# Optimization experiments

Hardware: AMD Instinct MI355X
Metric: run time of the kernel (lower is better)

## Reference

```python
import jax, jax.numpy as jnp
import numpy as np

N_NODES = 10000
N_EDGES = 80000
LATENT = 128
OUT_SIZE = 3
NODE_F = 12
EDGE_F = 7
STEPS = 15
LN_EPS = 1e-5


def _mlp(x, W0, b0, W1, b1, W2, b2):
    h = jax.nn.relu(x @ W0 + b0)
    h = jax.nn.relu(h @ W1 + b1)
    return h @ W2 + b2


def _ln(x, g, b):
    m = jnp.mean(x, axis=-1, keepdims=True)
    v = jnp.mean(jnp.square(x - m), axis=-1, keepdims=True)
    return (x - m) * jax.lax.rsqrt(v + LN_EPS) * g + b


def _forward(node_features, edge_features, senders, receivers,
             enW0, enb0, enW1, enb1, enW2, enb2, eng, enbe,
             eeW0, eeb0, eeW1, eeb1, eeW2, eeb2, eeg, eebe,
             beW0, beb0, beW1, beb1, beW2, beb2, beg, bebe,
             bnW0, bnb0, bnW1, bnb1, bnW2, bnb2, bng, bnbe,
             dW0, db0, dW1, db1, dW2, db2):
    # Encoder: node and mesh-edge MLPs with LayerNorm
    nl = _ln(_mlp(node_features, enW0, enb0, enW1, enb1, enW2, enb2), eng, enbe)  # [N, L]
    el = _ln(_mlp(edge_features, eeW0, eeb0, eeW1, eeb1, eeW2, eeb2), eeg, eebe)  # [E, L]

    # Processor: 15 GraphNetBlocks with residual connections, scanned over stacked params
    def block(carry, p):
        n, e = carry
        (eW0, eb0, eW1, eb1, eW2, eb2, eg, ebe,
         nW0, nb0, nW1, nb1, nW2, nb2, ng, nbe) = p
        feat = jnp.concatenate([n[senders], n[receivers], e], axis=-1)  # [E, 3L]
        new_e = _ln(_mlp(feat, eW0, eb0, eW1, eb1, eW2, eb2), eg, ebe)  # [E, L]
        agg = jax.ops.segment_sum(new_e, receivers, num_segments=N_NODES)  # [N, L]
        new_n = _ln(_mlp(jnp.concatenate([n, agg], axis=-1), nW0, nb0, nW1, nb1, nW2, nb2), ng, nbe)
        return (n + new_n, e + new_e), None

    xs = (beW0, beb0, beW1, beb1, beW2, beb2, beg, bebe,
          bnW0, bnb0, bnW1, bnb1, bnW2, bnb2, bng, bnbe)
    (nl, el), _ = jax.lax.scan(jax.checkpoint(block), (nl, el), xs)

    # Decoder: MLP without LayerNorm
    return _mlp(nl, dW0, db0, dW1, db1, dW2, db2)  # [N, OUT_SIZE]


def setup_inputs() -> dict:
    ks = iter(jax.random.split(jax.random.key(0), 32))

    def W(*shape):
        return jax.random.normal(next(ks), shape, jnp.float32) * (1.0 / np.sqrt(shape[-2]))

    z = lambda *s: jnp.zeros(s, jnp.float32)
    o = lambda *s: jnp.ones(s, jnp.float32)
    d = {}
    d['node_features'] = jax.random.normal(next(ks), (N_NODES, NODE_F), jnp.float32)
    d['edge_features'] = jax.random.normal(next(ks), (N_EDGES, EDGE_F), jnp.float32)
    d['senders'] = jax.random.randint(next(ks), (N_EDGES,), 0, N_NODES, jnp.int32)
    d['receivers'] = jax.random.randint(next(ks), (N_EDGES,), 0, N_NODES, jnp.int32)
    d.update(enW0=W(NODE_F, LATENT), enb0=z(LATENT), enW1=W(LATENT, LATENT), enb1=z(LATENT),
             enW2=W(LATENT, LATENT), enb2=z(LATENT), eng=o(LATENT), enbe=z(LATENT))
    d.update(eeW0=W(EDGE_F, LATENT), eeb0=z(LATENT), eeW1=W(LATENT, LATENT), eeb1=z(LATENT),
             eeW2=W(LATENT, LATENT), eeb2=z(LATENT), eeg=o(LATENT), eebe=z(LATENT))
    d.update(beW0=W(STEPS, 3 * LATENT, LATENT), beb0=z(STEPS, LATENT),
             beW1=W(STEPS, LATENT, LATENT), beb1=z(STEPS, LATENT),
             beW2=W(STEPS, LATENT, LATENT), beb2=z(STEPS, LATENT),
             beg=o(STEPS, LATENT), bebe=z(STEPS, LATENT))
    d.update(bnW0=W(STEPS, 2 * LATENT, LATENT), bnb0=z(STEPS, LATENT),
             bnW1=W(STEPS, LATENT, LATENT), bnb1=z(STEPS, LATENT),
             bnW2=W(STEPS, LATENT, LATENT), bnb2=z(STEPS, LATENT),
             bng=o(STEPS, LATENT), bnbe=z(STEPS, LATENT))
    d.update(dW0=W(LATENT, LATENT), db0=z(LATENT), dW1=W(LATENT, LATENT), db1=z(LATENT),
             dW2=W(LATENT, OUT_SIZE), db2=z(OUT_SIZE))
    return d


def reference(node_features, edge_features, senders, receivers,
              enW0, enb0, enW1, enb1, enW2, enb2, eng, enbe,
              eeW0, eeb0, eeW1, eeb1, eeW2, eeb2, eeg, eebe,
              beW0, beb0, beW1, beb1, beW2, beb2, beg, bebe,
              bnW0, bnb0, bnW1, bnb1, bnW2, bnb2, bng, bnbe,
              dW0, db0, dW1, db1, dW2, db2):
    return _forward(node_features, edge_features, senders, receivers,
                    enW0, enb0, enW1, enb1, enW2, enb2, eng, enbe,
                    eeW0, eeb0, eeW1, eeb1, eeW2, eeb2, eeg, eebe,
                    beW0, beb0, beW1, beb1, beW2, beb2, beg, bebe,
                    bnW0, bnb0, bnW1, bnb1, bnW2, bnb2, bng, bnbe,
                    dW0, db0, dW1, db1, dW2, db2)
```

## Files before the change

### kernel.cpp

```cpp
#include <hip/hip_runtime.h>
#include <hip/hip_bf16.h>
#include <stdint.h>

#define N_NODES 10000
#define N_EDGES 80000
#define L 128
#define STEPS 15
#define LN_EPS 1e-5f
#define NTHR 256
#define H_STRIDE 272

typedef short short8 __attribute__((ext_vector_type(8)));
typedef float floatx4 __attribute__((ext_vector_type(4)));

__device__ __forceinline__ float bf2f(const __hip_bfloat16 x) {
    return __bfloat162float(x);
}
__device__ __forceinline__ float ldmix(const void* p, int idx, int isf32) {
    return isf32 ? ((const float*)p)[idx]
                 : bf2f(((const __hip_bfloat16*)p)[idx]);
}

__global__ void detect_dtype(const uint32_t* __restrict__ nf, int* cnt) {
    int c = 0;
    for (int i = blockIdx.x * blockDim.x + threadIdx.x; i < 60000;
         i += gridDim.x * blockDim.x) {
        const uint32_t w = nf[i];
        c += (((w >> 7) & 0xFF) >= 0xC6) + (((w >> 23) & 0xFF) >= 0xC6);
    }
    atomicAdd(cnt, c);
}

#define N_TMATS 14
struct TAll {
    const void* src[N_TMATS];
    long long cum[N_TMATS + 1];
    int K[N_TMATS], N[N_TMATS], Kpad[N_TMATS];
};

__global__ void transpose_all(TAll a, const int* __restrict__ cnt,
                              __hip_bfloat16* __restrict__ pool) {
    const int isf32 = (*cnt > 1000);
    const long long total = a.cum[N_TMATS];
    for (long long i = blockIdx.x * (long long)blockDim.x + threadIdx.x;
         i < total; i += gridDim.x * (long long)blockDim.x) {
        int e = 0;
        #pragma unroll 1
        for (int j = 1; j < N_TMATS; j++) if (i >= a.cum[j]) e = j;
        const long long r = i - a.cum[e];
        const int per = a.N[e] * a.Kpad[e];
        const int m = (int)(r / per);
        int r2 = (int)(r - (long long)m * per);
        const int c2   = r2 >> 12;
        const int rem  = r2 & 4095;
        const int ct   = rem >> 9;
        const int lane = (rem >> 3) & 63;
        const int j    = rem & 7;
        const int k    = c2 * 32 + (lane >> 4) * 8 + j;
        const int col  = ct * 16 + (lane & 15);
        float v = 0.f;
        if (k < a.K[e]) v = ldmix(a.src[e], (m * a.K[e] + k) * a.N[e] + col, isf32);
        pool[i] = __float2bfloat16(v);
    }
}

__global__ void convert_feats(const void* __restrict__ nf,
                              const void* __restrict__ ef,
                              const int* __restrict__ cnt,
                              const int* __restrict__ elist,
                              __hip_bfloat16* __restrict__ fN,
                              __hip_bfloat16* __restrict__ fE)
{
    const int isf32 = (*cnt > 1000);
    const int totN = N_NODES * 32;
    const int totE = N_EDGES * 32;
    for (int i = blockIdx.x * blockDim.x + threadIdx.x; i < totN + totE;
         i += gridDim.x * blockDim.x) {
        if (i < totN) {
            const int r = i >> 5, c = i & 31;
            fN[i] = __float2bfloat16(c < 12 ? ldmix(nf, r * 12 + c, isf32) : 0.f);
        } else {
            const int j = i - totN;
            const int r = j >> 5, c = j & 31;
            const int e = elist[r];
            fE[j] = __float2bfloat16(c < 7 ? ldmix(ef, e * 7 + c, isf32) : 0.f);
        }
    }
}

__global__ void csr_hist(const int* __restrict__ rcv, int* __restrict__ deg) {
    for (int i = blockIdx.x * blockDim.x + threadIdx.x; i < N_EDGES;
         i += gridDim.x * blockDim.x)
        atomicAdd(&deg[rcv[i]], 1);
}

__global__ void csr_scan(const int* __restrict__ deg, int* __restrict__ rowptr,
                         int* __restrict__ cursor) {
    __shared__ int part[256];
    __shared__ int partx[257];
    const int t = threadIdx.x;
    int s = 0;
    for (int j = 0; j < 40; j++) {
        const int i = t * 40 + j;
        if (i < N_NODES) s += deg[i];
    }
    part[t] = s;
    __syncthreads();
    if (t == 0) {
        int r = 0;
        for (int k = 0; k < 256; k++) { partx[k] = r; r += part[k]; }
        partx[256] = r;
    }
    __syncthreads();
    int run = partx[t];
    for (int j = 0; j < 40; j++) {
        const int i = t * 40 + j;
        if (i < N_NODES) {
            rowptr[i] = run;
            cursor[i] = run;
            run += deg[i];
        }
    }
    if (t == 255) rowptr[N_NODES] = partx[256];
}

__global__ void csr_scatter(const int* __restrict__ rcv, int* __restrict__ cursor,
                            int* __restrict__ elist) {
    for (int i = blockIdx.x * blockDim.x + threadIdx.x; i < N_EDGES;
         i += gridDim.x * blockDim.x) {
        const int p = atomicAdd(&cursor[rcv[i]], 1);
        elist[p] = i;
    }
}

__global__ void sort_meta(const int* __restrict__ snd, const int* __restrict__ rcv,
                          const int* __restrict__ elist,
                          int* __restrict__ ssnd, int* __restrict__ srcv) {
    for (int i = blockIdx.x * blockDim.x + threadIdx.x; i < N_EDGES;
         i += gridDim.x * blockDim.x) {
        const int e = elist[i];
        ssnd[i] = snd[e];
        srcv[i] = rcv[e];
    }
}

__global__ __launch_bounds__(256)
void csr_agg(const int* __restrict__ rowptr,
             const __hip_bfloat16* __restrict__ ln16,
             __hip_bfloat16* __restrict__ agg16)
{
    const int g = threadIdx.x >> 5;
    const int lane = threadIdx.x & 31;
    const int v = blockIdx.x * 8 + g;
    if (v >= N_NODES) return;
    const int c0 = lane * 4;
    float s0 = 0.f, s1 = 0.f, s2 = 0.f, s3 = 0.f;
    int j = rowptr[v];
    const int en = rowptr[v + 1];
    for (; j + 1 < en; j += 2) {
        union { uint2 w; __hip_bfloat16 h[4]; } u0, u1;
        u0.w = *(const uint2*)(ln16 + (size_t)j * L + c0);
        u1.w = *(const uint2*)(ln16 + (size_t)(j + 1) * L + c0);
        s0 += bf2f(u0.h[0]); s1 += bf2f(u0.h[1]); s2 += bf2f(u0.h[2]); s3 += bf2f(u0.h[3]);
        s0 += bf2f(u1.h[0]); s1 += bf2f(u1.h[1]); s2 += bf2f(u1.h[2]); s3 += bf2f(u1.h[3]);
    }
    for (; j < en; j++) {
        union { uint2 w; __hip_bfloat16 h[4]; } u;
        u.w = *(const uint2*)(ln16 + (size_t)j * L + c0);
        s0 += bf2f(u.h[0]); s1 += bf2f(u.h[1]); s2 += bf2f(u.h[2]); s3 += bf2f(u.h[3]);
    }
    union { uint2 w; __hip_bfloat16 h[4]; } o;
    o.h[0] = __float2bfloat16(s0); o.h[1] = __float2bfloat16(s1);
    o.h[2] = __float2bfloat16(s2); o.h[3] = __float2bfloat16(s3);
    *(uint2*)(agg16 + (size_t)v * L + c0) = o.w;
}

enum AMode { A_PLAIN = 0, A_FEAT = 1, A_CAT = 2 };
enum Epi   { E_LN_STORE = 0, E_LN_EDGE = 1, E_LN_NODE = 2, E_DEC = 3 };

template <int AMODE, int EPI, int NL, int K0>
__global__ __launch_bounds__(NTHR, 3)
void fused_mlp(const __hip_bfloat16* __restrict__ A, int lda, int M,
               const __hip_bfloat16* __restrict__ WT0,
               const __hip_bfloat16* __restrict__ WT1,
               const __hip_bfloat16* __restrict__ WT2,
               const void* __restrict__ b0,
               const void* __restrict__ b1,
               const void* __restrict__ b2,
               const void* __restrict__ g,
               const void* __restrict__ beta,
               int poff,
               const int* __restrict__ cnt,
               const __hip_bfloat16* __restrict__ n16,
               const __hip_bfloat16* __restrict__ e16s,
               const __hip_bfloat16* __restrict__ agg16,
               const int* __restrict__ ssnd,
               const int* __restrict__ srcv,
               float* res32,
               __hip_bfloat16* res16,
               __hip_bfloat16* __restrict__ lnout,
               const void* __restrict__ dW,
               const void* __restrict__ db,
               void* __restrict__ dout)
{
    __shared__ __align__(16) char lds[17408 + 32768];
    char* wbuf = lds + 17408;

    const int tid  = threadIdx.x;
    const int wv   = tid >> 6;
    const int lane = tid & 63;
    const int quad = lane >> 4;
    const int m15  = lane & 15;
    const int row0 = blockIdx.x * 64;
    const int isf32 = (*cnt > 1000);

    char* hw = lds + wv * 4352;

    const int rw = row0 + wv * 16 + m15;
    const int rc = rw < M ? rw : M - 1;

    int sI = 0, rI = 0;
    if constexpr (AMODE == A_FEAT) { sI = ssnd[rc]; rI = srcv[rc]; }

    auto aFrag = [&](int kchunk) -> short8 {
        const int k0 = kchunk * 32 + quad * 8;
        const __hip_bfloat16* sp;
        if constexpr (AMODE == A_PLAIN) {
            sp = A + (size_t)rc * lda + k0;
        } else if constexpr (AMODE == A_FEAT) {
            if (k0 < L)          sp = n16  + (size_t)sI * L + k0;
            else if (k0 < 2 * L) sp = n16  + (size_t)rI * L + (k0 - L);
            else                 sp = e16s + (size_t)rc * L + (k0 - 2 * L);
        } else {
            if (k0 < L) sp = n16   + (size_t)rc * L + k0;
            else        sp = agg16 + (size_t)rc * L + (k0 - L);
        }
        return *(const short8*)sp;
    };
    auto loadW = [&](const __hip_bfloat16* secPtr, int ch, int4* wr) {
        #pragma unroll
        for (int it = 0; it < 4; it++)
            if (it < 2 * ch)
                wr[it] = *(const int4*)(secPtr + (size_t)wv * ch * 1024 + it * 512 + lane * 8);
    };
    auto storeW = [&](int buf, int ch, const int4* wr) {
        #pragma unroll
        for (int it = 0; it < 4; it++)
            if (it < 2 * ch)
                *(int4*)(wbuf + buf * 16384 + wv * ch * 2048 + it * 1024 + lane * 16) = wr[it];
    };
    auto bread = [&](int buf, int kc, int ct) -> short8 {
        return *(const short8*)(wbuf + buf * 16384 + kc * 8192 + ct * 1024 + lane * 16);
    };

    constexpr int CH0 = (K0 == 32) ? 1 : 2;
    constexpr int S0  = (K0 == 32) ? 1 : (K0 / 64);

    int4 wreg[4];
    short8 aF[2];
    int buf = 0;
    floatx4 acc[8];

    #pragma unroll
    for (int ct = 0; ct < 8; ct++) acc[ct] = (floatx4)0.f;

    loadW(WT0, CH0, wreg);
    aF[0] = aFrag(0);
    if constexpr (CH0 == 2) aF[1] = aFrag(1);

    for (int sec = 0; sec < S0; sec++) {
        storeW(buf, CH0, wreg);
        __syncthreads();
        const short8 a0 = aF[0];
        const short8 a1 = aF[1];
        if (sec + 1 < S0) {
            loadW(WT0 + (size_t)(sec + 1) * CH0 * 4096, CH0, wreg);
            aF[0] = aFrag((sec + 1) * CH0);
            if constexpr (CH0 == 2) aF[1] = aFrag((sec + 1) * CH0 + 1);
        } else {
            loadW(WT1, 2, wreg);
        }
        #pragma unroll
        for (int ct = 0; ct < 8; ct++)
            acc[ct] = __builtin_amdgcn_mfma_f32_16x16x32_bf16(a0, bread(buf, 0, ct), acc[ct], 0, 0, 0);
        if constexpr (CH0 == 2) {
            #pragma unroll
            for (int ct = 0; ct < 8; ct++)
                acc[ct] = __builtin_amdgcn_mfma_f32_16x16x32_bf16(a1, bread(buf, 1, ct), acc[ct], 0, 0, 0);
        }
        buf ^= 1;
    }
    {
        float bb[8];
        #pragma unroll
        for (int ct = 0; ct < 8; ct++) bb[ct] = ldmix(b0, poff + ct * 16 + m15, isf32);
        #pragma unroll
        for (int ct = 0; ct < 8; ct++)
            #pragma unroll
            for (int i = 0; i < 4; i++) {
                const int rl = quad * 4 + i;
                const int col = ct * 16 + m15;
                *(__hip_bfloat16*)(hw + rl * H_STRIDE + col * 2) =
                    __float2bfloat16(fmaxf(acc[ct][i] + bb[ct], 0.f));
            }
    }

    {
        #pragma unroll
        for (int ct = 0; ct < 8; ct++) acc[ct] = (floatx4)0.f;
        short8 af[4];
        #pragma unroll
        for (int c = 0; c < 4; c++)
            af[c] = *(const short8*)(hw + m15 * H_STRIDE + c * 64 + quad * 16);
        for (int sec = 0; sec < 2; sec++) {
            storeW(buf, 2, wreg);
            __syncthreads();
            if (sec == 0)            loadW(WT1 + 8192, 2, wreg);
            else if constexpr (NL == 3) loadW(WT2, 2, wreg);
            #pragma unroll
            for (int kc = 0; kc < 2; kc++)
                #pragma unroll
                for (int ct = 0; ct < 8; ct++)
                    acc[ct] = __builtin_amdgcn_mfma_f32_16x16x32_bf16(
                        af[sec * 2 + kc], bread(buf, kc, ct), acc[ct], 0, 0, 0);
            buf ^= 1;
        }
        float bb[8];
        #pragma unroll
        for (int ct = 0; ct < 8; ct++) bb[ct] = ldmix(b1, poff + ct * 16 + m15, isf32);
        #pragma unroll
        for (int ct = 0; ct < 8; ct++)
            #pragma unroll
            for (int i = 0; i < 4; i++) {
                const int rl = quad * 4 + i;
                const int col = ct * 16 + m15;
                *(__hip_bfloat16*)(hw + rl * H_STRIDE + col * 2) =
                    __float2bfloat16(fmaxf(acc[ct][i] + bb[ct], 0.f));
            }
    }

    if constexpr (NL == 3) {
        #pragma unroll
        for (int ct = 0; ct < 8; ct++) acc[ct] = (floatx4)0.f;
        short8 af[4];
        #pragma unroll
        for (int c = 0; c < 4; c++)
            af[c] = *(const short8*)(hw + m15 * H_STRIDE + c * 64 + quad * 16);
        for (int sec = 0; sec < 2; sec++) {
            storeW(buf, 2, wreg);
            __syncthreads();
            if (sec == 0) loadW(WT2 + 8192, 2, wreg);
            #pragma unroll
            for (int kc = 0; kc < 2; kc++)
                #pragma unroll
                for (int ct = 0; ct < 8; ct++)
                    acc[ct] = __builtin_amdgcn_mfma_f32_16x16x32_bf16(
                        af[sec * 2 + kc], bread(buf, kc, ct), acc[ct], 0, 0, 0);
            buf ^= 1;
        }
        float bb[8], gg[8], be[8];
        #pragma unroll
        for (int ct = 0; ct < 8; ct++) {
            bb[ct] = ldmix(b2,   poff + ct * 16 + m15, isf32);
            gg[ct] = ldmix(g,    poff + ct * 16 + m15, isf32);
            be[ct] = ldmix(beta, poff + ct * 16 + m15, isf32);
        }
        #pragma unroll
        for (int i = 0; i < 4; i++) {
            float t[8], s = 0.f, s2 = 0.f;
            #pragma unroll
            for (int ct = 0; ct < 8; ct++) {
                t[ct] = acc[ct][i] + bb[ct];
                s  += t[ct];
                s2 += t[ct] * t[ct];
            }
            #pragma unroll
            for (int m = 1; m < 16; m <<= 1) {
                s  += __shfl_xor(s,  m, 64);
                s2 += __shfl_xor(s2, m, 64);
            }
            const float mean = s * (1.f / 128.f);
            const float var  = s2 * (1.f / 128.f) - mean * mean;
            const float inv  = rsqrtf(fmaxf(var, 0.f) + LN_EPS);
            const int rg = row0 + wv * 16 + quad * 4 + i;
            if (rg < M) {
                #pragma unroll
                for (int ct = 0; ct < 8; ct++) {
                    const int col = ct * 16 + m15;
                    const float o = (t[ct] - mean) * inv * gg[ct] + be[ct];
                    const size_t idx = (size_t)rg * L + col;
                    if constexpr (EPI == E_LN_STORE) {
                        res32[idx] = o;
                        if (res16) res16[idx] = __float2bfloat16(o);
                    } else if constexpr (EPI == E_LN_NODE) {
                        const float nw = res32[idx] + o;
                        res32[idx] = nw;
                        res16[idx] = __float2bfloat16(nw);
                    } else {
                        const float nw = res32[idx] + o;
                        res32[idx] = nw;
                        res16[idx] = __float2bfloat16(nw);
                        lnout[idx] = __float2bfloat16(o);
                    }
                }
            }
        }
    } else {
        __syncthreads();
        float* Wl = (float*)wbuf;
        for (int i = tid; i < 3 * L; i += NTHR) {
            const int o = i / L, k = i - o * L;
            Wl[o * L + k] = ldmix(dW, k * 3 + o, isf32);
        }
        __syncthreads();
        if (tid < 64) {
            const int rg = row0 + tid;
            if (rg < M) {
                const __hip_bfloat16* hr =
                    (const __hip_bfloat16*)(lds + (tid >> 4) * 4352 + (tid & 15) * H_STRIDE);
                float s0 = ldmix(db, 0, isf32);
                float s1 = ldmix(db, 1, isf32);
                float s2 = ldmix(db, 2, isf32);
                #pragma unroll 8
                for (int k = 0; k < L; k++) {
                    const float hv = bf2f(hr[k]);
                    s0 += hv * Wl[k];
                    s1 += hv * Wl[L + k];
                    s2 += hv * Wl[2 * L + k];
                }
                if (isf32) {
                    float* o = (float*)dout;
                    o[rg * 3 + 0] = s0; o[rg * 3 + 1] = s1; o[rg * 3 + 2] = s2;
                } else {
                    __hip_bfloat16* o = (__hip_bfloat16*)dout;
                    o[rg * 3 + 0] = __float2bfloat16(s0);
                    o[rg * 3 + 1] = __float2bfloat16(s1);
                    o[rg * 3 + 2] = __float2bfloat16(s2);
                }
            }
        }
    }
}

extern "C" void kernel_launch(void* const* d_in, const int* in_sizes, int n_in,
                              void* d_out, int out_size, void* d_ws, size_t ws_size,
                              hipStream_t stream)
{
    (void)in_sizes; (void)n_in; (void)out_size; (void)ws_size;
    const int* snd = (const int*)d_in[2];
    const int* rcv = (const int*)d_in[3];

    char* ws = (char*)d_ws;
    int* cnt = (int*)ws;                              ws += 256;
    auto takeB = [&](size_t el) {
        __hip_bfloat16* p = (__hip_bfloat16*)ws;
        ws += ((el * 2 + 255) & ~255ull);
        return p;
    };
    auto takeF = [&](size_t el) {
        float* p = (float*)ws;
        ws += ((el * 4 + 255) & ~255ull);
        return p;
    };
    auto takeI = [&](size_t el) {
        int* p = (int*)ws;
        ws += ((el * 4 + 255) & ~255ull);
        return p;
    };

    const int srcIdx[N_TMATS] = {4, 6, 8, 12, 14, 16, 20, 22, 24, 28, 30, 32, 36, 38};
    const int tK[N_TMATS]    = {12, 128, 128, 7, 128, 128, 384, 128, 128, 256, 128, 128, 128, 128};
    const int tKp[N_TMATS]   = {32, 128, 128, 32, 128, 128, 384, 128, 128, 256, 128, 128, 128, 128};
    const int tNm[N_TMATS]   = {1, 1, 1, 1, 1, 1, STEPS, STEPS, STEPS, STEPS, STEPS, STEPS, 1, 1};
    TAll ta;
    long long cum = 0;
    __hip_bfloat16* wmat[N_TMATS];
    __hip_bfloat16* wpool = (__hip_bfloat16*)ws;
    for (int j = 0; j < N_TMATS; j++) {
        ta.src[j] = d_in[srcIdx[j]];
        ta.cum[j] = cum;
        ta.K[j] = tK[j]; ta.N[j] = 128; ta.Kpad[j] = tKp[j];
        wmat[j] = wpool + cum;
        cum += (long long)tNm[j] * 128 * tKp[j];
    }
    ta.cum[N_TMATS] = cum;
    ws += ((cum * 2 + 255) & ~255ull);

    float* n32 = takeF((size_t)N_NODES * L);
    float* e32 = takeF((size_t)N_EDGES * L);
    __hip_bfloat16* n16   = takeB((size_t)N_NODES * L);
    __hip_bfloat16* e16   = takeB((size_t)N_EDGES * L);
    __hip_bfloat16* ln16  = takeB((size_t)N_EDGES * L);
    __hip_bfloat16* agg16 = takeB((size_t)N_NODES * L);
    __hip_bfloat16* fN16  = takeB((size_t)N_NODES * 32);
    __hip_bfloat16* fE16  = takeB((size_t)N_EDGES * 32);
    int* deg    = takeI(N_NODES);
    int* rowptr = takeI(N_NODES + 1);
    int* cursor = takeI(N_NODES);
    int* elist  = takeI(N_EDGES);
    int* ssnd   = takeI(N_EDGES);
    int* srcv   = takeI(N_EDGES);

    const dim3 blk(NTHR);
    const dim3 grdE((N_EDGES + 63) / 64);
    const dim3 grdN((N_NODES + 63) / 64);

    (void)hipMemsetAsync(cnt, 0, sizeof(int), stream);
    (void)hipMemsetAsync(deg, 0, N_NODES * sizeof(int), stream);
    detect_dtype<<<dim3(64), blk, 0, stream>>>((const uint32_t*)d_in[0], cnt);
    transpose_all<<<dim3(512), blk, 0, stream>>>(ta, cnt, wpool);

    csr_hist<<<dim3(80), blk, 0, stream>>>(rcv, deg);
    csr_scan<<<dim3(1), blk, 0, stream>>>(deg, rowptr, cursor);
    csr_scatter<<<dim3(80), blk, 0, stream>>>(rcv, cursor, elist);
    sort_meta<<<dim3(80), blk, 0, stream>>>(snd, rcv, elist, ssnd, srcv);
    convert_feats<<<dim3(256), blk, 0, stream>>>(d_in[0], d_in[1], cnt, elist, fN16, fE16);

    fused_mlp<A_PLAIN, E_LN_STORE, 3, 32><<<grdE, blk, 0, stream>>>(
        fE16, 32, N_EDGES, wmat[3], wmat[4], wmat[5],
        d_in[13], d_in[15], d_in[17], d_in[18], d_in[19], 0, cnt,
        nullptr, nullptr, nullptr, nullptr, nullptr,
        e32, e16, nullptr, nullptr, nullptr, nullptr);
    fused_mlp<A_PLAIN, E_LN_STORE, 3, 32><<<grdN, blk, 0, stream>>>(
        fN16, 32, N_NODES, wmat[0], wmat[1], wmat[2],
        d_in[5], d_in[7], d_in[9], d_in[10], d_in[11], 0, cnt,
        nullptr, nullptr, nullptr, nullptr, nullptr,
        n32, n16, nullptr, nullptr, nullptr, nullptr);

    for (int s = 0; s < STEPS; s++) {
        const int po = s * L;
        fused_mlp<A_FEAT, E_LN_EDGE, 3, 384><<<grdE, blk, 0, stream>>>(
            nullptr, 0, N_EDGES,
            wmat[6] + (size_t)s * 128 * 384,
            wmat[7] + (size_t)s * 128 * 128,
            wmat[8] + (size_t)s * 128 * 128,
            d_in[21], d_in[23], d_in[25], d_in[26], d_in[27], po, cnt,
            n16, e16, nullptr, ssnd, srcv,
            e32, e16, ln16, nullptr, nullptr, nullptr);
        csr_agg<<<dim3((N_NODES + 7) / 8), blk, 0, stream>>>(rowptr, ln16, agg16);
        fused_mlp<A_CAT, E_LN_NODE, 3, 256><<<grdN, blk, 0, stream>>>(
            nullptr, 0, N_NODES,
            wmat[9]  + (size_t)s * 128 * 256,
            wmat[10] + (size_t)s * 128 * 128,
            wmat[11] + (size_t)s * 128 * 128,
            d_in[29], d_in[31], d_in[33], d_in[34], d_in[35], po, cnt,
            n16, nullptr, agg16, nullptr, nullptr,
            n32, n16, nullptr, nullptr, nullptr, nullptr);
    }

    fused_mlp<A_PLAIN, E_DEC, 2, 128><<<grdN, blk, 0, stream>>>(
        n16, 128, N_NODES, wmat[12], wmat[13], nullptr,
        d_in[37], d_in[39], nullptr, nullptr, nullptr, 0, cnt,
        nullptr, nullptr, nullptr, nullptr, nullptr,
        nullptr, nullptr, nullptr, d_in[40], d_in[41], d_out);
}
```

Baseline: 1.322 ms.

## Stage weights one 32-wide K chunk at a time to raise occupancy

Weight staging in the fused MLP kernel now moves one 32-row K chunk (8KB) per double-buffer slot instead of two chunks (16KB). This halves the weight LDS buffer and lets launch bounds request 4 blocks per CU instead of 3, with fewer registers held for prefetched weights. In exchange there are twice as many __syncthreads and LDS store/load rounds per layer, with less MFMA work between barriers to hide latency.

```diff
diff --git a/kernel.cpp b/kernel.cpp
--- a/kernel.cpp
+++ b/kernel.cpp
@@ -179,7 +179,7 @@
 enum Epi   { E_LN_STORE = 0, E_LN_EDGE = 1, E_LN_NODE = 2, E_DEC = 3 };
 
 template <int AMODE, int EPI, int NL, int K0>
-__global__ __launch_bounds__(NTHR, 3)
+__global__ __launch_bounds__(NTHR, 4)
 void fused_mlp(const __hip_bfloat16* __restrict__ A, int lda, int M,
                const __hip_bfloat16* __restrict__ WT0,
                const __hip_bfloat16* __restrict__ WT1,
@@ -203,7 +203,7 @@
                const void* __restrict__ db,
                void* __restrict__ dout)
 {
-    __shared__ __align__(16) char lds[17408 + 32768];
+    __shared__ __align__(16) char lds[17408 + 16384];
     char* wbuf = lds + 17408;
 
     const int tid  = threadIdx.x;
@@ -237,57 +237,44 @@
         }
         return *(const short8*)sp;
     };
-    auto loadW = [&](const __hip_bfloat16* secPtr, int ch, int4* wr) {
-        #pragma unroll
-        for (int it = 0; it < 4; it++)
-            if (it < 2 * ch)
-                wr[it] = *(const int4*)(secPtr + (size_t)wv * ch * 1024 + it * 512 + lane * 8);
-    };
-    auto storeW = [&](int buf, int ch, const int4* wr) {
-        #pragma unroll
-        for (int it = 0; it < 4; it++)
-            if (it < 2 * ch)
-                *(int4*)(wbuf + buf * 16384 + wv * ch * 2048 + it * 1024 + lane * 16) = wr[it];
-    };
-    auto bread = [&](int buf, int kc, int ct) -> short8 {
-        return *(const short8*)(wbuf + buf * 16384 + kc * 8192 + ct * 1024 + lane * 16);
-    };
-
-    constexpr int CH0 = (K0 == 32) ? 1 : 2;
-    constexpr int S0  = (K0 == 32) ? 1 : (K0 / 64);
-
-    int4 wreg[4];
-    short8 aF[2];
+    auto loadWc = [&](const __hip_bfloat16* base, int c, int4& x, int4& y) {
+        const __hip_bfloat16* p = base + (size_t)c * 4096 + tid * 16;
+        x = *(const int4*)p;
+        y = *(const int4*)(p + 8);
+    };
+    auto storeWc = [&](int b, const int4& x, const int4& y) {
+        *(int4*)(wbuf + b * 8192 + tid * 32)      = x;
+        *(int4*)(wbuf + b * 8192 + tid * 32 + 16) = y;
+    };
+    auto breadc = [&](int b, int ct) -> short8 {
+        return *(const short8*)(wbuf + b * 8192 + ct * 1024 + lane * 16);
+    };
+
+    constexpr int C0 = K0 / 32;
+
+    int4 w0, w1;
+    short8 aCur, aNext;
     int buf = 0;
     floatx4 acc[8];
 
     #pragma unroll
     for (int ct = 0; ct < 8; ct++) acc[ct] = (floatx4)0.f;
 
-    loadW(WT0, CH0, wreg);
-    aF[0] = aFrag(0);
-    if constexpr (CH0 == 2) aF[1] = aFrag(1);
-
-    for (int sec = 0; sec < S0; sec++) {
-        storeW(buf, CH0, wreg);
+    loadWc(WT0, 0, w0, w1);
+    aCur = aFrag(0);
+    if constexpr (C0 > 1) aNext = aFrag(1);
+
+    for (int c = 0; c < C0; c++) {
+        storeWc(buf, w0, w1);
         __syncthreads();
-        const short8 a0 = aF[0];
-        const short8 a1 = aF[1];
-        if (sec + 1 < S0) {
-            loadW(WT0 + (size_t)(sec + 1) * CH0 * 4096, CH0, wreg);
-            aF[0] = aFrag((sec + 1) * CH0);
-            if constexpr (CH0 == 2) aF[1] = aFrag((sec + 1) * CH0 + 1);
-        } else {
-            loadW(WT1, 2, wreg);
-        }
+        const short8 a = aCur;
+        aCur = aNext;
+        if (c + 2 < C0) aNext = aFrag(c + 2);
+        if (c + 1 < C0) loadWc(WT0, c + 1, w0, w1);
+        else            loadWc(WT1, 0, w0, w1);
         #pragma unroll
         for (int ct = 0; ct < 8; ct++)
-            acc[ct] = __builtin_amdgcn_mfma_f32_16x16x32_bf16(a0, bread(buf, 0, ct), acc[ct], 0, 0, 0);
-        if constexpr (CH0 == 2) {
-            #pragma unroll
-            for (int ct = 0; ct < 8; ct++)
-                acc[ct] = __builtin_amdgcn_mfma_f32_16x16x32_bf16(a1, bread(buf, 1, ct), acc[ct], 0, 0, 0);
-        }
+            acc[ct] = __builtin_amdgcn_mfma_f32_16x16x32_bf16(a, breadc(buf, ct), acc[ct], 0, 0, 0);
         buf ^= 1;
     }
     {
@@ -312,17 +299,14 @@
         #pragma unroll
         for (int c = 0; c < 4; c++)
             af[c] = *(const short8*)(hw + m15 * H_STRIDE + c * 64 + quad * 16);
-        for (int sec = 0; sec < 2; sec++) {
-            storeW(buf, 2, wreg);
+        for (int c = 0; c < 4; c++) {
+            storeWc(buf, w0, w1);
             __syncthreads();
-            if (sec == 0)            loadW(WT1 + 8192, 2, wreg);
-            else if constexpr (NL == 3) loadW(WT2, 2, wreg);
+            if (c < 3)               loadWc(WT1, c + 1, w0, w1);
+            else if constexpr (NL == 3) loadWc(WT2, 0, w0, w1);
             #pragma unroll
-            for (int kc = 0; kc < 2; kc++)
-                #pragma unroll
-                for (int ct = 0; ct < 8; ct++)
-                    acc[ct] = __builtin_amdgcn_mfma_f32_16x16x32_bf16(
-                        af[sec * 2 + kc], bread(buf, kc, ct), acc[ct], 0, 0, 0);
+            for (int ct = 0; ct < 8; ct++)
+                acc[ct] = __builtin_amdgcn_mfma_f32_16x16x32_bf16(af[c], breadc(buf, ct), acc[ct], 0, 0, 0);
             buf ^= 1;
         }
         float bb[8];
@@ -346,16 +330,13 @@
         #pragma unroll
         for (int c = 0; c < 4; c++)
             af[c] = *(const short8*)(hw + m15 * H_STRIDE + c * 64 + quad * 16);
-        for (int sec = 0; sec < 2; sec++) {
-            storeW(buf, 2, wreg);
+        for (int c = 0; c < 4; c++) {
+            storeWc(buf, w0, w1);
             __syncthreads();
-            if (sec == 0) loadW(WT2 + 8192, 2, wreg);
+            if (c < 3) loadWc(WT2, c + 1, w0, w1);
             #pragma unroll
-            for (int kc = 0; kc < 2; kc++)
-                #pragma unroll
-                for (int ct = 0; ct < 8; ct++)
-                    acc[ct] = __builtin_amdgcn_mfma_f32_16x16x32_bf16(
-                        af[sec * 2 + kc], bread(buf, kc, ct), acc[ct], 0, 0, 0);
+            for (int ct = 0; ct < 8; ct++)
+                acc[ct] = __builtin_amdgcn_mfma_f32_16x16x32_bf16(af[c], breadc(buf, ct), acc[ct], 0, 0, 0);
             buf ^= 1;
         }
         float bb[8], gg[8], be[8];
```

Result: slower. 1.464 ms (+10.8%).
